# Kernel optimization log

Measured on AMD Instinct MI355X. Metric: run time of the kernel, lower is better.

Reference implementation:

```python
import jax, jax.numpy as jnp
import numpy as np

B, T, S, O = 8, 60, 36, 1
H, E, PE = 4, 16, 16
AD, TA, OUT, L = 12, 10, 64, 2
PRUNE_KEEP_FROM = int(np.floor(S * S * 0.5))  # floor(S^2 * (1 - prune_rate))
EPS = 1e-5


def lrelu(v):
    return jax.nn.leaky_relu(v, 0.01)


def pos_encode(times):
    # standard sinusoidal PE on raw timestamps -> (B, T, PE)
    half = PE // 2
    div = jnp.exp(jnp.arange(half, dtype=jnp.float32) * (-jnp.log(10000.0) / half))
    ang = times[..., None] * div
    return jnp.stack([jnp.sin(ang), jnp.cos(ang)], axis=-1).reshape(times.shape + (PE,))


def pair_sim(adj):
    # sum_{i<j} ||a_i - a_j||^2 = B*sum_i||a_i||^2 - ||sum_i a_i||^2
    b = adj.shape[0]
    sq = jnp.sum(adj * adj)
    tot = jnp.sum(adj, axis=0)
    return (b * sq - jnp.sum(tot * tot)) / ((b - 1) ** 2) / (S * S)


def _forward(x, times, mask, bn_g, bn_b, obs_emb_w, attn_w, bidir_w, proj_W, proj_b,
             Wq, bq, Wk, bk, Ws, bs, lnt_g, lnt_b, Wse, bse, lns_g, lns_b):
    b = x.shape[0]
    # BatchNorm2d over timestep channels (training-mode batch stats)
    mu = x.mean(axis=(0, 2, 3), keepdims=True)
    var = x.var(axis=(0, 2, 3), keepdims=True)
    x = (x - mu) / jnp.sqrt(var + EPS) * bn_g[None, :, None, None] + bn_b[None, :, None, None]
    # per-sensor observation embedding: (B,T,S,O) x (S,O,E*H) -> (B,H,T,S,E)
    h = lrelu(jnp.einsum('btso,som->btsm', x, obs_emb_w))
    h = h.reshape(b, T, S, H, E).transpose(0, 3, 1, 2, 4)
    h = h * mask[:, None, :, :, None]
    pe = pos_encode(times)  # (B,T,PE)
    adj = jnp.ones((b, H, S, S), x.dtype)
    sim = pair_sim(adj)  # 0 for all-ones init, kept for faithfulness
    prune_msk = None
    for lay in range(L):
        hp = h @ proj_W.T + proj_b  # (B,H,T,S,AD+PE)
        cat = jnp.concatenate([
            jnp.broadcast_to(attn_w[lay][None, :, None], (b, H, T, S, AD)),
            jnp.broadcast_to(pe[:, None, :, None], (b, H, T, S, PE))], axis=-1)
        alpha = lrelu(jnp.einsum('bhtsd,bhtjd->bhtsj', hp, cat))  # (B,H,T,S,S)
        if lay:
            cnt = mask.sum(axis=1)[:, None, :, None]  # (B,1,S,1)
            adj = lrelu(adj * (alpha.sum(axis=2) / cnt))
            if prune_msk is None:
                flat = adj.reshape(b, H, S * S)
                ranks = jnp.argsort(jnp.argsort(flat, axis=-1), axis=-1)
                prune_msk = (ranks >= PRUNE_KEEP_FROM).astype(adj.dtype).reshape(b, H, S, S)
            adj = adj * prune_msk
            sim = sim + pair_sim(adj)
        bidir = lrelu(jnp.einsum('hsd,hjd->hsj', bidir_w[lay], bidir_w[lay]))  # (H,S,S)
        w = lrelu(bidir[None, :, None] * alpha * adj[:, :, None])  # (B,H,T,S,S)
        # broadcast message passing: (B,H,T,1,S,E) * (B,H,T,S,S,1) -> sum over source sensor
        h = lrelu(jnp.sum(lrelu(h[:, :, :, None, :, :] * w[..., None]), axis=4))
    pe_e = jnp.broadcast_to(pe[:, None, :, None], (b, H, T, S, PE))
    Hc = jnp.concatenate([h, pe_e], axis=-1).transpose(0, 1, 3, 2, 4)  # (B,H,S,T,E+PE)
    Q = Hc @ Wq.T + bq
    K = Hc @ Wk.T + bk
    beta = jnp.einsum('bhstd,bhsud->bhstu', Q, K)  # (B,H,S,T,T)
    beta = (beta @ Ws.T + bs)[..., 0]  # (B,H,S,T)
    m = beta.mean(axis=(-2, -1), keepdims=True)
    v = beta.var(axis=(-2, -1), keepdims=True)
    beta = (beta - m) / jnp.sqrt(v + EPS) * lnt_g + lnt_b
    out = lrelu(jnp.einsum('bhst,bhstd->bhsd', beta, Hc))
    out = lrelu(out @ Wse.T + bse)
    m2 = out.mean(axis=(-2, -1), keepdims=True)
    v2 = out.var(axis=(-2, -1), keepdims=True)
    out = (out - m2) / jnp.sqrt(v2 + EPS) * lns_g + lns_b
    out = out.transpose(0, 2, 1, 3).reshape(b, S, OUT)
    return out, sim


def setup_inputs():
    key = jax.random.key(0)
    ks = jax.random.split(key, 12)
    def rn(k, shape, scale=0.1):
        return jax.random.normal(k, shape, jnp.float32) * scale
    return {
        'x': jax.random.normal(ks[0], (B, T, S, O), jnp.float32),
        'times': jnp.tile(jnp.arange(T, dtype=jnp.float32), (B, 1)),
        'mask': jnp.ones((B, T, S), jnp.float32),
        'bn_g': jnp.ones((T,), jnp.float32),
        'bn_b': jnp.zeros((T,), jnp.float32),
        'obs_emb_w': rn(ks[1], (S, O, E * H)),
        'attn_w': rn(ks[2], (L, H, S, AD)),
        'bidir_w': rn(ks[3], (L, H, S, AD)),
        'proj_W': rn(ks[4], (AD + PE, E)),
        'proj_b': jnp.zeros((AD + PE,), jnp.float32),
        'Wq': rn(ks[5], (TA, E + PE)),
        'bq': jnp.zeros((TA,), jnp.float32),
        'Wk': rn(ks[6], (TA, E + PE)),
        'bk': jnp.zeros((TA,), jnp.float32),
        'Ws': rn(ks[7], (1, T)),
        'bs': jnp.zeros((1,), jnp.float32),
        'lnt_g': jnp.ones((S, T), jnp.float32),
        'lnt_b': jnp.zeros((S, T), jnp.float32),
        'Wse': rn(ks[8], (OUT // H, E + PE)),
        'bse': jnp.zeros((OUT // H,), jnp.float32),
        'lns_g': jnp.ones((S, OUT // H), jnp.float32),
        'lns_b': jnp.zeros((S, OUT // H), jnp.float32),
    }


def reference(x, times, mask, bn_g, bn_b, obs_emb_w, attn_w, bidir_w, proj_W, proj_b,
              Wq, bq, Wk, bk, Ws, bs, lnt_g, lnt_b, Wse, bse, lns_g, lns_b):
    return _forward(x, times, mask, bn_g, bn_b, obs_emb_w, attn_w, bidir_w, proj_W, proj_b,
                    Wq, bq, Wk, bk, Ws, bs, lnt_g, lnt_b, Wse, bse, lns_g, lns_b)
```

## Files before the change

kernel.cpp:

```cpp
#include <hip/hip_runtime.h>
#include <math.h>

#define Bc 8
#define Tc 60
#define Sc 36
#define Hc_ 4
#define Ec 16
#define PEc 16
#define ADc 12
#define TAc 10
#define OUTc 64
#define KEEP 648
#define EPSc 1e-5f
#define LOG1E4_8 1.15129254649702284f

#define WS_H2     18176
#define WS_H1     1124096
#define WS_ALPHA  2230016
#define WS_ADJ    4759808
#define WS_ADJP   4801280
#define WS_CNT    5050112
#define WS_PE     5050496
#define WS_BID1   5058176
#define WS_BETA   WS_ALPHA
#define WS_PART   (WS_ALPHA + 69120)
#define WS_OUT2   (WS_ALPHA + 71424)
#define WS_PART2  (WS_ALPHA + 89856)

__device__ __forceinline__ float lrelu(float v){ return fmaxf(v, 0.01f*v); }
__device__ __forceinline__ float4 lrelu4(float4 v){
    return make_float4(lrelu(v.x), lrelu(v.y), lrelu(v.z), lrelu(v.w));
}

__global__ __launch_bounds__(256) void k_layer01(const float* __restrict__ x,
                          const float* __restrict__ times,
                          const float* __restrict__ mask,
                          const float* __restrict__ bn_g,
                          const float* __restrict__ bn_b,
                          const float* __restrict__ obs_w,
                          const float* __restrict__ attn,
                          const float* __restrict__ bidw,
                          const float* __restrict__ projW,
                          const float* __restrict__ projb,
                          float* __restrict__ ws){
    int idx = blockIdx.x;
    int t = idx % Tc; int bh = idx / Tc; int h = bh % Hc_; int b = bh / Hc_;
    int tid = threadIdx.x;
    __shared__ __align__(16) float sh_h[Sc*Ec];
    __shared__ __align__(16) float sh_h1[Sc*Ec];
    __shared__ float sh_pe[PEc];
    __shared__ __align__(16) float sh_at0T[ADc*Sc];
    __shared__ __align__(16) float sh_at1T[ADc*Sc];
    __shared__ __align__(16) float sh_bwT[ADc*Sc];
    __shared__ float sh_hp[Sc*28];
    __shared__ __align__(16) float sh_w[Sc*Sc];
    __shared__ float sh_xn[Sc];
    __shared__ float sh_m[Sc];
    __shared__ float sred[8];
    float s0 = 0.f, s1 = 0.f;
    for (int i = tid; i < Bc*Sc; i += 256){
        float v = x[((i/Sc)*Tc + t)*Sc + (i%Sc)];
        s0 += v; s1 += v*v;
    }
    #pragma unroll
    for (int off = 32; off; off >>= 1){
        s0 += __shfl_down(s0, off, 64);
        s1 += __shfl_down(s1, off, 64);
    }
    if ((tid & 63) == 0){ sred[(tid>>6)*2] = s0; sred[(tid>>6)*2 + 1] = s1; }
    if (tid >= 64 && tid < 80){
        int q = tid - 64; int j = q >> 1;
        float ang = times[b*Tc + t] * expf(-(float)j * LOG1E4_8);
        float pv = (q & 1) ? cosf(ang) : sinf(ang);
        sh_pe[q] = pv;
        if (h == 0) ws[WS_PE + (b*Tc + t)*PEc + q] = pv;
    }
    for (int i = tid; i < ADc*Sc; i += 256){
        int d = i / Sc, j = i % Sc;
        sh_at0T[i] = attn[h*Sc*ADc + j*ADc + d];
        sh_at1T[i] = attn[(Hc_ + h)*Sc*ADc + j*ADc + d];
        sh_bwT[i]  = bidw[h*Sc*ADc + j*ADc + d];
    }
    __syncthreads();
    float mu  = (sred[0]+sred[2]+sred[4]+sred[6]) / (float)(Bc*Sc);
    float var = (sred[1]+sred[3]+sred[5]+sred[7]) / (float)(Bc*Sc) - mu*mu;
    if (tid < Sc){
        float xv = x[(b*Tc + t)*Sc + tid];
        sh_xn[tid] = (xv - mu) * rsqrtf(var + EPSc) * bn_g[t] + bn_b[t];
        sh_m[tid]  = mask[(b*Tc + t)*Sc + tid];
    }
    __syncthreads();
    for (int i2 = tid; i2 < 288; i2 += 256){
        int s = i2 >> 3, e0 = (i2 & 7) << 1;
        float2 ow = *(const float2*)(obs_w + s*64 + h*Ec + e0);
        float xn = sh_xn[s], mm = sh_m[s];
        float2 r;
        r.x = lrelu(xn*ow.x)*mm; r.y = lrelu(xn*ow.y)*mm;
        *(float2*)(sh_h + s*Ec + e0) = r;
    }
    __syncthreads();
    for (int i = tid; i < Sc*28; i += 256){
        int s = i / 28, d = i % 28;
        const float4* hh4 = (const float4*)(sh_h + s*Ec);
        const float4* w4  = (const float4*)(projW + d*Ec);
        float acc = projb[d];
        #pragma unroll
        for (int q = 0; q < 4; q++){
            float4 hv = hh4[q], wv = w4[q];
            acc += hv.x*wv.x; acc += hv.y*wv.y; acc += hv.z*wv.z; acc += hv.w*wv.w;
        }
        sh_hp[i] = acc;
    }
    __syncthreads();
    for (int i4 = tid; i4 < 324; i4 += 256){
        int s = i4 / 9, j0 = (i4 % 9) << 2;
        const float* hp = sh_hp + s*28;
        float ps = 0.f;
        #pragma unroll
        for (int d = 0; d < PEc; d++) ps += hp[ADc + d]*sh_pe[d];
        float4 acc = make_float4(ps, ps, ps, ps);
        float4 bd = make_float4(0.f, 0.f, 0.f, 0.f);
        #pragma unroll
        for (int d = 0; d < ADc; d++){
            float hpd = hp[d];
            float4 a = *(const float4*)(sh_at0T + d*Sc + j0);
            acc.x += hpd*a.x; acc.y += hpd*a.y; acc.z += hpd*a.z; acc.w += hpd*a.w;
            float bws = sh_bwT[d*Sc + s];
            float4 bj = *(const float4*)(sh_bwT + d*Sc + j0);
            bd.x += bws*bj.x; bd.y += bws*bj.y; bd.z += bws*bj.z; bd.w += bws*bj.w;
        }
        float4 r;
        r.x = lrelu(lrelu(bd.x)*lrelu(acc.x));
        r.y = lrelu(lrelu(bd.y)*lrelu(acc.y));
        r.z = lrelu(lrelu(bd.z)*lrelu(acc.z));
        r.w = lrelu(lrelu(bd.w)*lrelu(acc.w));
        *(float4*)(sh_w + s*Sc + j0) = r;
    }
    __syncthreads();
    float* h1g = ws + WS_H1 + (size_t)idx*Sc*Ec;
    for (int i2 = tid; i2 < 288; i2 += 256){
        int s = i2 >> 3, e0 = (i2 & 7) << 1;
        float2 acc = make_float2(0.f, 0.f);
        const float* wr = sh_w + s*Sc;
        #pragma unroll 6
        for (int j = 0; j < Sc; j++){
            float2 hv = *(const float2*)(sh_h + j*Ec + e0);
            float w = wr[j];
            acc.x += lrelu(hv.x*w); acc.y += lrelu(hv.y*w);
        }
        float2 v; v.x = lrelu(acc.x); v.y = lrelu(acc.y);
        *(float2*)(sh_h1 + s*Ec + e0) = v;
        *(float2*)(h1g + s*Ec + e0) = v;
    }
    __syncthreads();
    for (int i = tid; i < Sc*28; i += 256){
        int s = i / 28, d = i % 28;
        const float4* hh4 = (const float4*)(sh_h1 + s*Ec);
        const float4* w4  = (const float4*)(projW + d*Ec);
        float acc = projb[d];
        #pragma unroll
        for (int q = 0; q < 4; q++){
            float4 hv = hh4[q], wv = w4[q];
            acc += hv.x*wv.x; acc += hv.y*wv.y; acc += hv.z*wv.z; acc += hv.w*wv.w;
        }
        sh_hp[i] = acc;
    }
    __syncthreads();
    float* adst = ws + WS_ALPHA + (size_t)idx*Sc*Sc;
    for (int i4 = tid; i4 < 324; i4 += 256){
        int s = i4 / 9, j0 = (i4 % 9) << 2;
        const float* hp = sh_hp + s*28;
        float ps = 0.f;
        #pragma unroll
        for (int d = 0; d < PEc; d++) ps += hp[ADc + d]*sh_pe[d];
        float4 acc = make_float4(ps, ps, ps, ps);
        #pragma unroll
        for (int d = 0; d < ADc; d++){
            float hpd = hp[d];
            float4 a = *(const float4*)(sh_at1T + d*Sc + j0);
            acc.x += hpd*a.x; acc.y += hpd*a.y; acc.z += hpd*a.z; acc.w += hpd*a.w;
        }
        *(float4*)(adst + s*Sc + j0) = lrelu4(acc);
    }
}

__global__ __launch_bounds__(256) void k_adjpart(const float* __restrict__ mask,
                                                 const float* __restrict__ bidw,
                                                 float* __restrict__ ws){
    int blk = blockIdx.x;
    int quar = blk & 3; int chunk = (blk >> 2) % 6; int bh = blk / 24;
    int tid = threadIdx.x;
    const float4* a = (const float4*)(ws + WS_ALPHA + (size_t)bh*Tc*Sc*Sc) + (size_t)chunk*10*324;
    float4* p = (float4*)(ws + WS_ADJP + (size_t)(bh*6 + chunk)*Sc*Sc);
    for (int c = quar*81 + tid; c < quar*81 + 81; c += 256){
        float4 acc = make_float4(0.f, 0.f, 0.f, 0.f);
        #pragma unroll
        for (int tt = 0; tt < 10; tt++){
            float4 u = a[(size_t)tt*324 + c];
            acc.x += u.x; acc.y += u.y; acc.z += u.z; acc.w += u.w;
        }
        p[c] = acc;
    }
    if (chunk == 0 && quar == 0 && (bh & 3) == 0 && tid < Sc){
        int b = bh >> 2;
        float c = 0.f;
        #pragma unroll 4
        for (int t = 0; t < Tc; t++) c += mask[(b*Tc + t)*Sc + tid];
        ws[WS_CNT + b*Sc + tid] = c;
    }
    if (chunk == 5 && quar == 1 && bh < Hc_){
        int h = bh;
        const float* bw = bidw + (Hc_ + h)*Sc*ADc;
        for (int i = tid; i < Sc*Sc; i += 256){
            int s = i / Sc, j = i % Sc;
            float bd = 0.f;
            #pragma unroll
            for (int d = 0; d < ADc; d++) bd += bw[s*ADc + d]*bw[j*ADc + d];
            ws[WS_BID1 + h*Sc*Sc + i] = lrelu(bd);
        }
    }
}

__global__ __launch_bounds__(256) void k_prune(float* __restrict__ ws){
    int bh = blockIdx.x / 24; int chunk = blockIdx.x % 24;
    int b = bh >> 2;
    int tid = threadIdx.x;
    __shared__ __align__(16) float sh_v[Sc*Sc];
    __shared__ float sh_cnt[Sc];
    const float4* p = (const float4*)(ws + WS_ADJP + (size_t)bh*6*Sc*Sc);
    for (int c = tid; c < 324; c += 256){
        float4 acc = make_float4(0.f, 0.f, 0.f, 0.f);
        #pragma unroll
        for (int q = 0; q < 6; q++){
            float4 u = p[(size_t)q*324 + c];
            acc.x += u.x; acc.y += u.y; acc.z += u.z; acc.w += u.w;
        }
        ((float4*)sh_v)[c] = acc;
    }
    if (tid < Sc) sh_cnt[tid] = ws[WS_CNT + b*Sc + tid];
    __syncthreads();
    for (int i = tid; i < Sc*Sc; i += 256){
        int s = i / Sc;
        sh_v[i] = lrelu(sh_v[i] / sh_cnt[s]);
    }
    __syncthreads();
    int r = tid >> 2; if (r > 53) r = 53;
    int part = tid & 3;
    int i = chunk*54 + r;
    float v = sh_v[i];
    const float4* v4 = (const float4*)sh_v + part*81;
    int a0 = part*324;
    int cnt = 0;
    #pragma unroll 9
    for (int j = 0; j < 81; j++){
        float4 u = v4[j];
        int k = a0 + j*4;
        cnt += (int)(u.x < v) + ((int)(u.x == v) & (int)(k   < i));
        cnt += (int)(u.y < v) + ((int)(u.y == v) & (int)(k+1 < i));
        cnt += (int)(u.z < v) + ((int)(u.z == v) & (int)(k+2 < i));
        cnt += (int)(u.w < v) + ((int)(u.w == v) & (int)(k+3 < i));
    }
    cnt += __shfl_down(cnt, 2, 4);
    cnt += __shfl_down(cnt, 1, 4);
    if (part == 0 && tid < 216)
        ws[WS_ADJ + bh*Sc*Sc + i] = (cnt >= KEEP) ? v : 0.f;
}

__global__ __launch_bounds__(256) void k_layer1mp(float* __restrict__ ws){
    int idx = blockIdx.x;
    int t = idx % Tc; int bh = idx / Tc; int h = bh % Hc_;
    int tid = threadIdx.x;
    __shared__ __align__(16) float sh_h[Sc*Ec];
    __shared__ __align__(16) float sh_w[Sc*Sc];
    const float4* hsrc4 = (const float4*)(ws + WS_H1 + (size_t)idx*Sc*Ec);
    const float4* al4  = (const float4*)(ws + WS_ALPHA + (size_t)idx*Sc*Sc);
    const float4* adj4 = (const float4*)(ws + WS_ADJ + bh*Sc*Sc);
    const float4* gbd4 = (const float4*)(ws + WS_BID1 + h*Sc*Sc);
    for (int i4 = tid; i4 < 144; i4 += 256) ((float4*)sh_h)[i4] = hsrc4[i4];
    for (int i4 = tid; i4 < 324; i4 += 256){
        float4 g = gbd4[i4], a = al4[i4], ad = adj4[i4];
        float4 r;
        r.x = lrelu(g.x*a.x*ad.x); r.y = lrelu(g.y*a.y*ad.y);
        r.z = lrelu(g.z*a.z*ad.z); r.w = lrelu(g.w*a.w*ad.w);
        ((float4*)sh_w)[i4] = r;
    }
    __syncthreads();
    for (int i2 = tid; i2 < 288; i2 += 256){
        int s = i2 >> 3, e0 = (i2 & 7) << 1;
        float2 acc = make_float2(0.f, 0.f);
        const float* wr = sh_w + s*Sc;
        #pragma unroll 6
        for (int j = 0; j < Sc; j++){
            float2 hv = *(const float2*)(sh_h + j*Ec + e0);
            float w = wr[j];
            acc.x += lrelu(hv.x*w); acc.y += lrelu(hv.y*w);
        }
        float2 v; v.x = lrelu(acc.x); v.y = lrelu(acc.y);
        *(float2*)(ws + WS_H2 + ((size_t)(bh*Sc + s)*Tc + t)*Ec + e0) = v;
    }
}

__global__ __launch_bounds__(256) void kF1(const float* __restrict__ Wq, const float* __restrict__ bq,
                   const float* __restrict__ Wk, const float* __restrict__ bk,
                   const float* __restrict__ Ws_, const float* __restrict__ bs_,
                   float* __restrict__ ws){
    int idx = blockIdx.x;
    int bh = idx / Sc; int b = bh / Hc_;
    int tid = threadIdx.x;
    __shared__ float sh_Hc[Tc*33];
    __shared__ float sh_K[Tc*11];
    __shared__ float sh_Wq[TAc*32];
    __shared__ float sh_WkT[32*TAc];
    __shared__ float sh_bq[TAc], sh_bk[TAc];
    __shared__ float sh_ws[Tc];
    __shared__ float sh_Kw[TAc];
    __shared__ float sh_wv[32];
    __shared__ float sh_c0;
    const float* h2c = ws + WS_H2 + (size_t)idx*Tc*Ec;
    for (int i4 = tid; i4 < Tc*4; i4 += 256){
        int t = i4 >> 2, c4 = i4 & 3;
        float4 u = *(const float4*)(h2c + i4*4);
        float* d = sh_Hc + t*33 + c4*4;
        d[0] = u.x; d[1] = u.y; d[2] = u.z; d[3] = u.w;
    }
    for (int i4 = tid; i4 < Tc*4; i4 += 256){
        int t = i4 >> 2, c4 = i4 & 3;
        float4 u = *(const float4*)(ws + WS_PE + (size_t)(b*Tc + t)*PEc + c4*4);
        float* d = sh_Hc + t*33 + Ec + c4*4;
        d[0] = u.x; d[1] = u.y; d[2] = u.z; d[3] = u.w;
    }
    for (int i = tid; i < TAc*32; i += 256){
        sh_Wq[i] = Wq[i];
        int d = i / 32, q = i % 32;
        sh_WkT[q*TAc + d] = Wk[i];
    }
    if (tid < TAc){ sh_bq[tid] = bq[tid]; sh_bk[tid] = bk[tid]; }
    if (tid < Tc) sh_ws[tid] = Ws_[tid];
    __syncthreads();
    for (int i = tid; i < Tc*TAc; i += 256){
        int t = i / TAc, d = i % TAc;
        const float* hc = sh_Hc + t*33;
        float acc = sh_bk[d];
        #pragma unroll
        for (int q = 0; q < 32; q++) acc += hc[q]*sh_WkT[q*TAc + d];
        sh_K[t*11 + d] = acc;
    }
    __syncthreads();
    if (tid < TAc){
        float acc = 0.f;
        #pragma unroll 4
        for (int t = 0; t < Tc; t++) acc += sh_K[t*11 + tid]*sh_ws[t];
        sh_Kw[tid] = acc;
    }
    __syncthreads();
    if (tid < 32){
        float acc = 0.f;
        #pragma unroll
        for (int d = 0; d < TAc; d++) acc += sh_Wq[d*32 + tid]*sh_Kw[d];
        sh_wv[tid] = acc;
    }
    if (tid == 32){
        float acc = 0.f;
        #pragma unroll
        for (int d = 0; d < TAc; d++) acc += sh_bq[d]*sh_Kw[d];
        sh_c0 = acc;
    }
    __syncthreads();
    if (tid < 64){
        float bv = 0.f;
        if (tid < Tc){
            const float* hc = sh_Hc + tid*33;
            float acc = bs_[0] + sh_c0;
            #pragma unroll
            for (int q = 0; q < 32; q++) acc += hc[q]*sh_wv[q];
            bv = acc;
            ws[WS_BETA + idx*Tc + tid] = acc;
        }
        float p0 = (tid < Tc) ? bv : 0.f;
        float p1 = p0*bv;
        #pragma unroll
        for (int off = 32; off; off >>= 1){
            p0 += __shfl_down(p0, off, 64);
            p1 += __shfl_down(p1, off, 64);
        }
        if (tid == 0){
            ws[WS_PART + idx*2]     = p0;
            ws[WS_PART + idx*2 + 1] = p1;
        }
    }
}

__global__ __launch_bounds__(256) void kF2(const float* __restrict__ lnt_g, const float* __restrict__ lnt_b,
                   const float* __restrict__ Wse, const float* __restrict__ bse,
                   float* __restrict__ ws){
    int idx = blockIdx.x;
    int s = idx % Sc; int bh = idx / Sc; int b = bh / Hc_;
    int tid = threadIdx.x;
    __shared__ float sh_Hc[Tc*33];
    __shared__ float sh_beta[Tc];
    __shared__ float sh_o1[32];
    __shared__ float sh_mi[2];
    if (tid < 64){
        float p0 = 0.f, p1 = 0.f;
        if (tid < Sc){
            p0 = ws[WS_PART + (bh*Sc + tid)*2];
            p1 = ws[WS_PART + (bh*Sc + tid)*2 + 1];
        }
        #pragma unroll
        for (int off = 32; off; off >>= 1){
            p0 += __shfl_down(p0, off, 64);
            p1 += __shfl_down(p1, off, 64);
        }
        if (tid == 0){
            float m = p0 / (float)(Sc*Tc);
            sh_mi[0] = m;
            sh_mi[1] = rsqrtf(p1 / (float)(Sc*Tc) - m*m + EPSc);
        }
    }
    const float* h2c = ws + WS_H2 + (size_t)idx*Tc*Ec;
    for (int i4 = tid; i4 < Tc*4; i4 += 256){
        int t = i4 >> 2, c4 = i4 & 3;
        float4 u = *(const float4*)(h2c + i4*4);
        float* d = sh_Hc + t*33 + c4*4;
        d[0] = u.x; d[1] = u.y; d[2] = u.z; d[3] = u.w;
    }
    for (int i4 = tid; i4 < Tc*4; i4 += 256){
        int t = i4 >> 2, c4 = i4 & 3;
        float4 u = *(const float4*)(ws + WS_PE + (size_t)(b*Tc + t)*PEc + c4*4);
        float* d = sh_Hc + t*33 + Ec + c4*4;
        d[0] = u.x; d[1] = u.y; d[2] = u.z; d[3] = u.w;
    }
    __syncthreads();
    float m = sh_mi[0], inv = sh_mi[1];
    if (tid < Tc){
        float bvv = ws[WS_BETA + idx*Tc + tid];
        sh_beta[tid] = (bvv - m)*inv*lnt_g[s*Tc + tid] + lnt_b[s*Tc + tid];
    }
    __syncthreads();
    if (tid < 32){
        float acc = 0.f;
        #pragma unroll 4
        for (int t = 0; t < Tc; t++) acc += sh_beta[t]*sh_Hc[t*33 + tid];
        sh_o1[tid] = lrelu(acc);
    }
    __syncthreads();
    if (tid < 64){
        float v = 0.f;
        if (tid < 16){
            float acc = bse[tid];
            const float* w = Wse + tid*32;
            #pragma unroll
            for (int d = 0; d < 32; d++) acc += sh_o1[d]*w[d];
            v = lrelu(acc);
            ws[WS_OUT2 + idx*16 + tid] = v;
        }
        float q0 = v, q1 = v*v;
        #pragma unroll
        for (int off = 32; off; off >>= 1){
            q0 += __shfl_down(q0, off, 64);
            q1 += __shfl_down(q1, off, 64);
        }
        if (tid == 0){
            ws[WS_PART2 + idx*2]     = q0;
            ws[WS_PART2 + idx*2 + 1] = q1;
        }
    }
}

__global__ __launch_bounds__(256) void kF3s(const float* __restrict__ lns_g, const float* __restrict__ lns_b,
                    const float* __restrict__ ws, float* __restrict__ out){
    int tid = threadIdx.x;
    if (blockIdx.x == 32){
        float sq = 0.f, t2 = 0.f;
        for (int i = tid; i < Hc_*Sc*Sc; i += 256){
            float tot = 0.f;
            #pragma unroll
            for (int b = 0; b < Bc; b++){
                float v = ws[WS_ADJ + b*Hc_*Sc*Sc + i];
                sq += v*v; tot += v;
            }
            t2 += tot*tot;
        }
        __shared__ float r0[256], r1[256];
        r0[tid] = sq; r1[tid] = t2; __syncthreads();
        for (int off = 128; off; off >>= 1){
            if (tid < off){ r0[tid] += r0[tid+off]; r1[tid] += r1[tid+off]; }
            __syncthreads();
        }
        if (tid == 0)
            out[Bc*Sc*OUTc] = ((float)Bc*r0[0] - r1[0]) / 49.f / 1296.f;
        return;
    }
    int bh = blockIdx.x; int h = bh % Hc_; int b = bh / Hc_;
    __shared__ float sh_mi[2];
    if (tid < 64){
        float p0 = 0.f, p1 = 0.f;
        if (tid < Sc){
            p0 = ws[WS_PART2 + (bh*Sc + tid)*2];
            p1 = ws[WS_PART2 + (bh*Sc + tid)*2 + 1];
        }
        #pragma unroll
        for (int off = 32; off; off >>= 1){
            p0 += __shfl_down(p0, off, 64);
            p1 += __shfl_down(p1, off, 64);
        }
        if (tid == 0){
            float m = p0 / (float)(Sc*16);
            sh_mi[0] = m;
            sh_mi[1] = rsqrtf(p1 / (float)(Sc*16) - m*m + EPSc);
        }
    }
    __syncthreads();
    float m2 = sh_mi[0], inv2 = sh_mi[1];
    for (int i = tid; i < Sc*16; i += 256){
        int s = i / 16, k = i % 16;
        float v = ws[WS_OUT2 + bh*Sc*16 + i];
        out[(b*Sc + s)*OUTc + h*16 + k] = (v - m2)*inv2*lns_g[i] + lns_b[i];
    }
}

extern "C" void kernel_launch(void* const* d_in, const int* in_sizes, int n_in,
                              void* d_out, int out_size, void* d_ws, size_t ws_size,
                              hipStream_t stream){
    const float* x     = (const float*)d_in[0];
    const float* times = (const float*)d_in[1];
    const float* mask  = (const float*)d_in[2];
    const float* bn_g  = (const float*)d_in[3];
    const float* bn_b  = (const float*)d_in[4];
    const float* obs   = (const float*)d_in[5];
    const float* attn  = (const float*)d_in[6];
    const float* bidw  = (const float*)d_in[7];
    const float* projW = (const float*)d_in[8];
    const float* projb = (const float*)d_in[9];
    const float* Wq    = (const float*)d_in[10];
    const float* bq    = (const float*)d_in[11];
    const float* Wk    = (const float*)d_in[12];
    const float* bk    = (const float*)d_in[13];
    const float* Ws_   = (const float*)d_in[14];
    const float* bs_   = (const float*)d_in[15];
    const float* lnt_g = (const float*)d_in[16];
    const float* lnt_b = (const float*)d_in[17];
    const float* Wse   = (const float*)d_in[18];
    const float* bse   = (const float*)d_in[19];
    const float* lns_g = (const float*)d_in[20];
    const float* lns_b = (const float*)d_in[21];
    float* ws  = (float*)d_ws;
    float* out = (float*)d_out;

    k_layer01<<<Bc*Hc_*Tc, 256, 0, stream>>>(x, times, mask, bn_g, bn_b, obs, attn, bidw, projW, projb, ws);
    k_adjpart<<<Bc*Hc_*24, 256, 0, stream>>>(mask, bidw, ws);
    k_prune<<<Bc*Hc_*24, 256, 0, stream>>>(ws);
    k_layer1mp<<<Bc*Hc_*Tc, 256, 0, stream>>>(ws);
    kF1<<<Bc*Hc_*Sc, 256, 0, stream>>>(Wq, bq, Wk, bk, Ws_, bs_, ws);
    kF2<<<Bc*Hc_*Sc, 256, 0, stream>>>(lnt_g, lnt_b, Wse, bse, ws);
    kF3s<<<Bc*Hc_ + 1, 256, 0, stream>>>(lns_g, lns_b, ws, out);
}
```

Baseline: 182.9 us.

## Fuse layer-1 message passing into temporal attention kernel

Merges k_layer1mp into kF1, so each (b,h,s) block computes its own h2 rows across all timesteps and keeps them in shared memory, saving one launch and an h2 reread. The key projection is rewritten algebraically: instead of computing K for every timestep and then weighting by Ws, the block first takes the Ws-weighted sum of the hidden states and projects once. The beta/part buffers move out of the alpha region because alpha is still being read in the fused kernel. Block indices are swizzled, and the alpha and h1 reads now use strided gathers with less reuse.

```diff
diff --git a/kernel.cpp b/kernel.cpp
--- a/kernel.cpp
+++ b/kernel.cpp
@@ -22,10 +22,10 @@
 #define WS_CNT    5050112
 #define WS_PE     5050496
 #define WS_BID1   5058176
-#define WS_BETA   WS_ALPHA
-#define WS_PART   (WS_ALPHA + 69120)
-#define WS_OUT2   (WS_ALPHA + 71424)
-#define WS_PART2  (WS_ALPHA + 89856)
+#define WS_BETA   5063424
+#define WS_PART   (WS_BETA + 69120)
+#define WS_OUT2   (WS_PART + 2304)
+#define WS_PART2  (WS_OUT2 + 18432)
 
 __device__ __forceinline__ float lrelu(float v){ return fmaxf(v, 0.01f*v); }
 __device__ __forceinline__ float4 lrelu4(float4 v){
@@ -266,90 +266,85 @@
         ws[WS_ADJ + bh*Sc*Sc + i] = (cnt >= KEEP) ? v : 0.f;
 }
 
-__global__ __launch_bounds__(256) void k_layer1mp(float* __restrict__ ws){
-    int idx = blockIdx.x;
-    int t = idx % Tc; int bh = idx / Tc; int h = bh % Hc_;
-    int tid = threadIdx.x;
-    __shared__ __align__(16) float sh_h[Sc*Ec];
-    __shared__ __align__(16) float sh_w[Sc*Sc];
-    const float4* hsrc4 = (const float4*)(ws + WS_H1 + (size_t)idx*Sc*Ec);
-    const float4* al4  = (const float4*)(ws + WS_ALPHA + (size_t)idx*Sc*Sc);
-    const float4* adj4 = (const float4*)(ws + WS_ADJ + bh*Sc*Sc);
-    const float4* gbd4 = (const float4*)(ws + WS_BID1 + h*Sc*Sc);
-    for (int i4 = tid; i4 < 144; i4 += 256) ((float4*)sh_h)[i4] = hsrc4[i4];
-    for (int i4 = tid; i4 < 324; i4 += 256){
-        float4 g = gbd4[i4], a = al4[i4], ad = adj4[i4];
-        float4 r;
-        r.x = lrelu(g.x*a.x*ad.x); r.y = lrelu(g.y*a.y*ad.y);
-        r.z = lrelu(g.z*a.z*ad.z); r.w = lrelu(g.w*a.w*ad.w);
-        ((float4*)sh_w)[i4] = r;
-    }
-    __syncthreads();
-    for (int i2 = tid; i2 < 288; i2 += 256){
-        int s = i2 >> 3, e0 = (i2 & 7) << 1;
-        float2 acc = make_float2(0.f, 0.f);
-        const float* wr = sh_w + s*Sc;
-        #pragma unroll 6
-        for (int j = 0; j < Sc; j++){
-            float2 hv = *(const float2*)(sh_h + j*Ec + e0);
-            float w = wr[j];
-            acc.x += lrelu(hv.x*w); acc.y += lrelu(hv.y*w);
-        }
-        float2 v; v.x = lrelu(acc.x); v.y = lrelu(acc.y);
-        *(float2*)(ws + WS_H2 + ((size_t)(bh*Sc + s)*Tc + t)*Ec + e0) = v;
-    }
-}
-
-__global__ __launch_bounds__(256) void kF1(const float* __restrict__ Wq, const float* __restrict__ bq,
+__global__ __launch_bounds__(256) void kF1m(const float* __restrict__ Wq, const float* __restrict__ bq,
                    const float* __restrict__ Wk, const float* __restrict__ bk,
                    const float* __restrict__ Ws_, const float* __restrict__ bs_,
                    float* __restrict__ ws){
-    int idx = blockIdx.x;
-    int bh = idx / Sc; int b = bh / Hc_;
+    int idx = (blockIdx.x & 7)*144 + (blockIdx.x >> 3);
+    int s = idx % Sc; int bh = idx / Sc; int h = bh % Hc_; int b = bh / Hc_;
     int tid = threadIdx.x;
-    __shared__ float sh_Hc[Tc*33];
-    __shared__ float sh_K[Tc*11];
+    __shared__ float sh_Hc[Tc*34];
+    __shared__ float sh_w[Tc*Sc];
+    __shared__ float sh_bd[Sc];
+    __shared__ float sh_adj[Sc];
     __shared__ float sh_Wq[TAc*32];
     __shared__ float sh_WkT[32*TAc];
     __shared__ float sh_bq[TAc], sh_bk[TAc];
     __shared__ float sh_ws[Tc];
+    __shared__ float sh_hw[32];
+    __shared__ float sh_Sws;
     __shared__ float sh_Kw[TAc];
     __shared__ float sh_wv[32];
     __shared__ float sh_c0;
-    const float* h2c = ws + WS_H2 + (size_t)idx*Tc*Ec;
-    for (int i4 = tid; i4 < Tc*4; i4 += 256){
-        int t = i4 >> 2, c4 = i4 & 3;
-        float4 u = *(const float4*)(h2c + i4*4);
-        float* d = sh_Hc + t*33 + c4*4;
-        d[0] = u.x; d[1] = u.y; d[2] = u.z; d[3] = u.w;
-    }
     for (int i4 = tid; i4 < Tc*4; i4 += 256){
         int t = i4 >> 2, c4 = i4 & 3;
         float4 u = *(const float4*)(ws + WS_PE + (size_t)(b*Tc + t)*PEc + c4*4);
-        float* d = sh_Hc + t*33 + Ec + c4*4;
+        float* d = sh_Hc + t*34 + Ec + c4*4;
         d[0] = u.x; d[1] = u.y; d[2] = u.z; d[3] = u.w;
+    }
+    if (tid >= 64 && tid < 64 + Sc){
+        int j = tid - 64;
+        sh_bd[j]  = ws[WS_BID1 + h*Sc*Sc + s*Sc + j];
+        sh_adj[j] = ws[WS_ADJ + bh*Sc*Sc + s*Sc + j];
     }
     for (int i = tid; i < TAc*32; i += 256){
         sh_Wq[i] = Wq[i];
         int d = i / 32, q = i % 32;
         sh_WkT[q*TAc + d] = Wk[i];
     }
-    if (tid < TAc){ sh_bq[tid] = bq[tid]; sh_bk[tid] = bk[tid]; }
-    if (tid < Tc) sh_ws[tid] = Ws_[tid];
-    __syncthreads();
-    for (int i = tid; i < Tc*TAc; i += 256){
-        int t = i / TAc, d = i % TAc;
-        const float* hc = sh_Hc + t*33;
-        float acc = sh_bk[d];
-        #pragma unroll
-        for (int q = 0; q < 32; q++) acc += hc[q]*sh_WkT[q*TAc + d];
-        sh_K[t*11 + d] = acc;
-    }
-    __syncthreads();
-    if (tid < TAc){
+    if (tid >= 128 && tid < 128 + TAc){ sh_bq[tid-128] = bq[tid-128]; sh_bk[tid-128] = bk[tid-128]; }
+    if (tid >= 192 && tid < 192 + Tc) sh_ws[tid-192] = Ws_[tid-192];
+    __syncthreads();
+    const float* al = ws + WS_ALPHA + (size_t)bh*Tc*Sc*Sc + s*Sc;
+    for (int i = tid; i < Tc*Sc; i += 256){
+        int t = i / Sc, j = i % Sc;
+        sh_w[i] = lrelu(sh_bd[j]*al[(size_t)t*Sc*Sc + j]*sh_adj[j]);
+    }
+    __syncthreads();
+    const float* h1 = ws + WS_H1 + (size_t)bh*Tc*Sc*Ec;
+    float* h2 = ws + WS_H2 + (size_t)idx*Tc*Ec;
+    for (int i2 = tid; i2 < 480; i2 += 256){
+        int t = i2 >> 3, e0 = (i2 & 7) << 1;
+        float2 acc = make_float2(0.f, 0.f);
+        const float* hr = h1 + (size_t)t*Sc*Ec + e0;
+        const float* wr = sh_w + t*Sc;
+        #pragma unroll 6
+        for (int j = 0; j < Sc; j++){
+            float2 hv = *(const float2*)(hr + j*Ec);
+            float w = wr[j];
+            acc.x += lrelu(hv.x*w); acc.y += lrelu(hv.y*w);
+        }
+        float2 v; v.x = lrelu(acc.x); v.y = lrelu(acc.y);
+        *(float2*)(sh_Hc + t*34 + e0) = v;
+        *(float2*)(h2 + t*Ec + e0) = v;
+    }
+    __syncthreads();
+    if (tid < 32){
         float acc = 0.f;
         #pragma unroll 4
-        for (int t = 0; t < Tc; t++) acc += sh_K[t*11 + tid]*sh_ws[t];
+        for (int t = 0; t < Tc; t++) acc += sh_ws[t]*sh_Hc[t*34 + tid];
+        sh_hw[tid] = acc;
+    } else if (tid == 32){
+        float acc = 0.f;
+        #pragma unroll 4
+        for (int t = 0; t < Tc; t++) acc += sh_ws[t];
+        sh_Sws = acc;
+    }
+    __syncthreads();
+    if (tid < TAc){
+        float acc = sh_bk[tid]*sh_Sws;
+        #pragma unroll
+        for (int q = 0; q < 32; q++) acc += sh_hw[q]*sh_WkT[q*TAc + tid];
         sh_Kw[tid] = acc;
     }
     __syncthreads();
@@ -358,8 +353,7 @@
         #pragma unroll
         for (int d = 0; d < TAc; d++) acc += sh_Wq[d*32 + tid]*sh_Kw[d];
         sh_wv[tid] = acc;
-    }
-    if (tid == 32){
+    } else if (tid == 32){
         float acc = 0.f;
         #pragma unroll
         for (int d = 0; d < TAc; d++) acc += sh_bq[d]*sh_Kw[d];
@@ -369,7 +363,7 @@
     if (tid < 64){
         float bv = 0.f;
         if (tid < Tc){
-            const float* hc = sh_Hc + tid*33;
+            const float* hc = sh_Hc + tid*34;
             float acc = bs_[0] + sh_c0;
             #pragma unroll
             for (int q = 0; q < 32; q++) acc += hc[q]*sh_wv[q];
@@ -550,8 +544,7 @@
     k_layer01<<<Bc*Hc_*Tc, 256, 0, stream>>>(x, times, mask, bn_g, bn_b, obs, attn, bidw, projW, projb, ws);
     k_adjpart<<<Bc*Hc_*24, 256, 0, stream>>>(mask, bidw, ws);
     k_prune<<<Bc*Hc_*24, 256, 0, stream>>>(ws);
-    k_layer1mp<<<Bc*Hc_*Tc, 256, 0, stream>>>(ws);
-    kF1<<<Bc*Hc_*Sc, 256, 0, stream>>>(Wq, bq, Wk, bk, Ws_, bs_, ws);
+    kF1m<<<Bc*Hc_*Sc, 256, 0, stream>>>(Wq, bq, Wk, bk, Ws_, bs_, ws);
     kF2<<<Bc*Hc_*Sc, 256, 0, stream>>>(lnt_g, lnt_b, Wse, bse, ws);
     kF3s<<<Bc*Hc_ + 1, 256, 0, stream>>>(lns_g, lns_b, ws, out);
 }
```

Result: slower. 200.5 us (+9.6%).
